# Kernel tuning notes

Hardware: AMD Instinct MI355X
Metric: run time of the kernel (lower is better)

## Reference

```python
import jax, jax.numpy as jnp
import numpy as np

H = 1024
NH = 16
DH = H // NH
EPS = 1e-12


def _heads(x):
    # [B,T,H] -> [B,NH,T,DH]
    B, T, _ = x.shape
    return x.reshape(B, T, NH, DH).transpose(0, 2, 1, 3)


def _layernorm(x, g, b):
    mu = jnp.mean(x, axis=-1, keepdims=True)
    var = jnp.mean(jnp.square(x - mu), axis=-1, keepdims=True)
    return (x - mu) * jax.lax.rsqrt(var + EPS) * g + b


def setup_inputs() -> dict:
    key = jax.random.key(0)
    ks = jax.random.split(key, 24)
    B, Tw, Te = 4, 1024, 128
    s = 0.02
    inp = {
        "word_hidden_states": jax.random.normal(ks[0], (B, Tw, H), jnp.float32),
        "entity_hidden_states": jax.random.normal(ks[1], (B, Te, H), jnp.float32),
        "attention_mask": jnp.zeros((B, 1, 1, Tw + Te), jnp.float32),
        "query_pos": jax.random.normal(ks[2], (B, Te, H), jnp.float32),
    }
    names = ["Wq", "Wk", "Wv", "Weq", "Wek", "Wev", "Wo", "Weo"]
    for i, n in enumerate(names):
        inp[n] = jax.random.normal(ks[3 + i], (H, H), jnp.float32) * s
        inp["b" + n[1:]] = jnp.zeros((H,), jnp.float32)
    inp["ln_g"] = jnp.ones((H,), jnp.float32)
    inp["ln_b"] = jnp.zeros((H,), jnp.float32)
    inp["eln_g"] = jnp.ones((H,), jnp.float32)
    inp["eln_b"] = jnp.zeros((H,), jnp.float32)
    return inp


def reference(word_hidden_states, entity_hidden_states, attention_mask, query_pos,
              Wq, bq, Wk, bk, Wv, bv, Weq, beq, Wek, bek, Wev, bev,
              Wo, bo, Weo, beo, ln_g, ln_b, eln_g, eln_b):
    Tw = word_hidden_states.shape[1]
    pos_ent = (entity_hidden_states + query_pos) * 0.5

    # per-stream projections (entity stream has its own e2w projections)
    qw = _heads(word_hidden_states @ Wq + bq)      # [B,NH,Tw,DH]
    qe = _heads(pos_ent @ Weq + beq)               # [B,NH,Te,DH]
    kw = _heads(word_hidden_states @ Wk + bk)
    ke = _heads(pos_ent @ Wek + bek)
    vw = _heads(word_hidden_states @ Wv + bv)
    ve = _heads(entity_hidden_states @ Wev + bev)  # value uses raw entity states

    q = jnp.concatenate([qw, qe], axis=2)          # [B,NH,T,DH]
    k = jnp.concatenate([kw, ke], axis=2)
    v = jnp.concatenate([vw, ve], axis=2)

    scores = jnp.einsum("bhqd,bhkd->bhqk", q, k) / np.sqrt(DH).astype(np.float32)
    scores = scores + attention_mask
    probs = jax.nn.softmax(scores, axis=-1)
    ctx = jnp.einsum("bhqk,bhkd->bhqd", probs, v)  # [B,NH,T,DH]
    B, _, T, _ = ctx.shape
    ctx = ctx.transpose(0, 2, 1, 3).reshape(B, T, H)

    word_self = ctx[:, :Tw, :]
    ent_self = ctx[:, Tw:, :]

    word_out = _layernorm(word_self @ Wo + bo + word_hidden_states, ln_g, ln_b)
    ent_out = _layernorm(ent_self @ Weo + beo + entity_hidden_states, eln_g, eln_b)
    return (word_out, ent_out)
```

## Files before the change

### kernel.cpp

```cpp
#include <hip/hip_runtime.h>
#include <math.h>

#define H_DIM 1024
#define NHEAD 16
#define DHEAD 64
#define T_W 1024
#define T_E 128
#define T_T 1152
#define BATCH 4

typedef __attribute__((ext_vector_type(8))) short s8b;
typedef __attribute__((ext_vector_type(4))) short s4b;
typedef __attribute__((ext_vector_type(4))) float f32x4;

__device__ __forceinline__ unsigned short f2bf(float f) {
    unsigned int u = __float_as_uint(f);
    u = (u + 0x7fffu + ((u >> 16) & 1u)) >> 16;
    return (unsigned short)u;
}

__device__ __forceinline__ void gld_lds16(const void* g, void* l) {
    __builtin_amdgcn_global_load_lds(
        (const __attribute__((address_space(1))) unsigned int*)g,
        (__attribute__((address_space(3))) unsigned int*)l, 16, 0, 0);
}

__global__ __launch_bounds__(256) void k_prep(const float* __restrict__ word,
                                              const float* __restrict__ ent,
                                              const float* __restrict__ qp,
                                              unsigned short* __restrict__ word_bf,
                                              unsigned short* __restrict__ pe_bf,
                                              unsigned short* __restrict__ ent_bf) {
    const int bid = blockIdx.x;
    if (bid < 4096) {
        int i = bid * 256 + threadIdx.x;
        float4 v = ((const float4*)word)[i];
        s4b o; o[0] = (short)f2bf(v.x); o[1] = (short)f2bf(v.y);
        o[2] = (short)f2bf(v.z); o[3] = (short)f2bf(v.w);
        *(s4b*)(word_bf + (size_t)i * 4) = o;
    } else {
        int i = (bid - 4096) * 256 + threadIdx.x;
        float4 a = ((const float4*)ent)[i];
        float4 b = ((const float4*)qp)[i];
        s4b e; e[0] = (short)f2bf(a.x); e[1] = (short)f2bf(a.y);
        e[2] = (short)f2bf(a.z); e[3] = (short)f2bf(a.w);
        *(s4b*)(ent_bf + (size_t)i * 4) = e;
        s4b p;
        p[0] = (short)f2bf((a.x + b.x) * 0.5f);
        p[1] = (short)f2bf((a.y + b.y) * 0.5f);
        p[2] = (short)f2bf((a.z + b.z) * 0.5f);
        p[3] = (short)f2bf((a.w + b.w) * 0.5f);
        *(s4b*)(pe_bf + (size_t)i * 4) = p;
    }
}

struct WPtrs { const float* w[8]; };
__global__ __launch_bounds__(256) void k_wT8(WPtrs ws, unsigned short* __restrict__ dstall) {
    __shared__ float tile[32][33];
    const float* src = ws.w[blockIdx.z];
    unsigned short* dst = dstall + (size_t)blockIdx.z * H_DIM * H_DIM;
    const int tx = threadIdx.x & 31, ty = threadIdx.x >> 5;
    const int kb = blockIdx.x * 32, nb = blockIdx.y * 32;
    #pragma unroll
    for (int i = 0; i < 4; i++)
        tile[ty * 4 + i][tx] = src[(size_t)(kb + ty * 4 + i) * H_DIM + nb + tx];
    __syncthreads();
    #pragma unroll
    for (int i = 0; i < 4; i++)
        dst[(size_t)(nb + ty * 4 + i) * H_DIM + kb + tx] = f2bf(tile[tx][ty * 4 + i]);
}

struct B3 { const float* b[3]; };
struct O3 { void* o[3]; };

__global__ __launch_bounds__(256) void k_proj(
    const unsigned short* __restrict__ A0, const unsigned short* __restrict__ A2,
    const unsigned short* __restrict__ Wtbase, B3 biases, O3 outs,
    int Tseq, int toff)
{
    const int z = blockIdx.z;
    const unsigned short* A = (z == 2) ? A2 : A0;
    const unsigned short* B = Wtbase + (size_t)z * H_DIM * H_DIM;
    const float* bias = biases.b[z];
    void* outp = outs.o[z];

    __shared__ unsigned short sm[8192];
    const int t = threadIdx.x;
    const int w = t >> 6, lane = t & 63;
    const int col = lane & 15, quad = lane >> 4;
    const int m0 = blockIdx.y * 128, n0 = blockIdx.x * 128;
    const int wm = w & 1, wn = w >> 1;
    const int rA = t >> 2, kA = (t & 3) * 8;

    f32x4 acc[4][4] = {};

    const unsigned short* gA0 = A + (size_t)(m0 + rA) * H_DIM + kA;
    const unsigned short* gA1 = A + (size_t)(m0 + 64 + rA) * H_DIM + kA;
    const unsigned short* gB0 = B + (size_t)(n0 + rA) * H_DIM + kA;
    const unsigned short* gB1 = B + (size_t)(n0 + 64 + rA) * H_DIM + kA;
    unsigned short* lA0 = &sm[t * 8];
    unsigned short* lA1 = &sm[2048 + t * 8];
    unsigned short* lB0 = &sm[4096 + t * 8];
    unsigned short* lB1 = &sm[6144 + t * 8];

    for (int k0 = 0; k0 < H_DIM; k0 += 32) {
        gld_lds16(gA0 + k0, lA0);
        gld_lds16(gA1 + k0, lA1);
        gld_lds16(gB0 + k0, lB0);
        gld_lds16(gB1 + k0, lB1);
        __syncthreads();
        s8b af[4], bfr[4];
        #pragma unroll
        for (int mt = 0; mt < 4; mt++)
            af[mt] = *(const s8b*)&sm[(wm * 64 + mt * 16 + col) * 32 + quad * 8];
        #pragma unroll
        for (int nt = 0; nt < 4; nt++)
            bfr[nt] = *(const s8b*)&sm[4096 + (wn * 64 + nt * 16 + col) * 32 + quad * 8];
        #pragma unroll
        for (int mt = 0; mt < 4; mt++)
            #pragma unroll
            for (int nt = 0; nt < 4; nt++)
                acc[mt][nt] = __builtin_amdgcn_mfma_f32_16x16x32_bf16(
                    af[mt], bfr[nt], acc[mt][nt], 0, 0, 0);
        __syncthreads();
    }

    #pragma unroll
    for (int mt = 0; mt < 4; mt++) {
        const int mg = m0 + wm * 64 + mt * 16 + quad * 4;
        const int b = mg / Tseq, tt = toff + (mg % Tseq);
        #pragma unroll
        for (int nt = 0; nt < 4; nt++) {
            const int ng = n0 + wn * 64 + nt * 16 + col;
            f32x4 c = acc[mt][nt];
            const float bn = bias[ng];
            if (z < 2) {
                unsigned short* out = (unsigned short*)outp;
                #pragma unroll
                for (int r = 0; r < 4; r++)
                    out[((size_t)b * T_T + tt + r) * H_DIM + ng] = f2bf(c[r] + bn);
            } else {
                unsigned short* out = (unsigned short*)outp;
                #pragma unroll
                for (int r = 0; r < 4; r++)
                    out[((size_t)b * H_DIM + ng) * T_T + tt + r] = f2bf(c[r] + bn);
            }
        }
    }
}

__global__ __launch_bounds__(256) void k_gemm_out(
    const unsigned short* __restrict__ ctx,
    const unsigned short* __restrict__ Wt_o, const unsigned short* __restrict__ Wt_eo,
    const float* __restrict__ bo, const float* __restrict__ beo,
    const float* __restrict__ word, const float* __restrict__ ent,
    float* __restrict__ out_word, float* __restrict__ out_ent)
{
    const int blk = blockIdx.x;
    const bool is_word = blk < 256;
    const int lb = is_word ? blk : blk - 256;
    const int m0 = (lb >> 3) * 128, n0 = (lb & 7) * 128;
    const unsigned short* B = is_word ? Wt_o : Wt_eo;
    const float* bias = is_word ? bo : beo;
    const float* resid = is_word ? word : ent;
    float* out = is_word ? out_word : out_ent;
    const int Tseq = is_word ? T_W : T_E;
    const int toff = is_word ? 0 : T_W;

    __shared__ unsigned short sm[8192];
    const int t = threadIdx.x;
    const int w = t >> 6, lane = t & 63;
    const int col = lane & 15, quad = lane >> 4;
    const int wm = w & 1, wn = w >> 1;
    const int rA = t >> 2, kA = (t & 3) * 8;

    f32x4 acc[4][4] = {};

    const int r0 = m0 + rA, r1 = m0 + 64 + rA;
    const size_t arow0 = (size_t)(r0 / Tseq) * T_T + toff + (r0 % Tseq);
    const size_t arow1 = (size_t)(r1 / Tseq) * T_T + toff + (r1 % Tseq);
    const unsigned short* gA0 = ctx + arow0 * H_DIM + kA;
    const unsigned short* gA1 = ctx + arow1 * H_DIM + kA;
    const unsigned short* gB0 = B + (size_t)(n0 + rA) * H_DIM + kA;
    const unsigned short* gB1 = B + (size_t)(n0 + 64 + rA) * H_DIM + kA;
    unsigned short* lA0 = &sm[t * 8];
    unsigned short* lA1 = &sm[2048 + t * 8];
    unsigned short* lB0 = &sm[4096 + t * 8];
    unsigned short* lB1 = &sm[6144 + t * 8];

    for (int k0 = 0; k0 < H_DIM; k0 += 32) {
        gld_lds16(gA0 + k0, lA0);
        gld_lds16(gA1 + k0, lA1);
        gld_lds16(gB0 + k0, lB0);
        gld_lds16(gB1 + k0, lB1);
        __syncthreads();
        s8b af[4], bfr[4];
        #pragma unroll
        for (int mt = 0; mt < 4; mt++)
            af[mt] = *(const s8b*)&sm[(wm * 64 + mt * 16 + col) * 32 + quad * 8];
        #pragma unroll
        for (int nt = 0; nt < 4; nt++)
            bfr[nt] = *(const s8b*)&sm[4096 + (wn * 64 + nt * 16 + col) * 32 + quad * 8];
        #pragma unroll
        for (int mt = 0; mt < 4; mt++)
            #pragma unroll
            for (int nt = 0; nt < 4; nt++)
                acc[mt][nt] = __builtin_amdgcn_mfma_f32_16x16x32_bf16(
                    af[mt], bfr[nt], acc[mt][nt], 0, 0, 0);
        __syncthreads();
    }

    #pragma unroll
    for (int mt = 0; mt < 4; mt++) {
        const int mg = m0 + wm * 64 + mt * 16 + quad * 4;
        #pragma unroll
        for (int nt = 0; nt < 4; nt++) {
            const int ng = n0 + wn * 64 + nt * 16 + col;
            f32x4 c = acc[mt][nt];
            const float bn = bias[ng];
            #pragma unroll
            for (int r = 0; r < 4; r++) {
                const size_t idx = (size_t)(mg + r) * H_DIM + ng;
                out[idx] = c[r] + bn + resid[idx];
            }
        }
    }
}

__global__ __launch_bounds__(256) void k_attn(
    const unsigned short* __restrict__ q, const unsigned short* __restrict__ k,
    const unsigned short* __restrict__ vt, const float* __restrict__ mask,
    unsigned short* __restrict__ ctx)
{
    const int tid = threadIdx.x;
    const int w = tid >> 6, lane = tid & 63;
    const int col = lane & 15, quad = lane >> 4;
    const int bh = blockIdx.x / 18;
    const int q0 = (blockIdx.x % 18) * 64 + w * 16;
    const int b = bh >> 4, h = bh & 15;

    __shared__ unsigned short sK[2][64 * 64];
    __shared__ unsigned short sV[2][64 * 64];
    __shared__ __align__(16) unsigned short sP[4][16 * 64];
    unsigned short* sp = &sP[w][0];

    const unsigned short* qp = q + ((size_t)b * T_T + q0) * H_DIM + h * DHEAD;
    const unsigned short* kp = k + (size_t)b * T_T * H_DIM + h * DHEAD;
    const unsigned short* vp = vt + ((size_t)b * H_DIM + h * DHEAD) * T_T;
    const float* mp = mask + (size_t)b * T_T;

    const s8b qf0 = *(const s8b*)(qp + (size_t)col * H_DIM + quad * 8);
    const s8b qf1 = *(const s8b*)(qp + (size_t)col * H_DIM + 32 + quad * 8);

    const int rA = tid >> 3;
    const int cA = (tid & 7) ^ (rA & 7);

    f32x4 O[4] = {};
    float m_c = -1e30f, l_c = 0.f;

    #define PREFETCH(J0, BUF)                                                        \
        {                                                                            \
            unsigned short* dK = &sK[BUF][0];                                        \
            unsigned short* dV = &sV[BUF][0];                                        \
            gld_lds16(kp + (size_t)((J0) + rA) * H_DIM + cA * 8, dK + tid * 8);      \
            gld_lds16(kp + (size_t)((J0) + rA + 32) * H_DIM + cA * 8,                \
                      dK + (256 + tid) * 8);                                         \
            gld_lds16(vp + (size_t)rA * T_T + (J0) + cA * 8, dV + tid * 8);          \
            gld_lds16(vp + (size_t)(rA + 32) * T_T + (J0) + cA * 8,                  \
                      dV + (256 + tid) * 8);                                         \
        }

    PREFETCH(0, 0)
    for (int it = 0; it < 18; it++) {
        const int j0 = it * 64;
        __syncthreads();
        if (it < 17) PREFETCH(j0 + 64, (it + 1) & 1)
        const unsigned short* K0 = &sK[it & 1][0];
        const unsigned short* V0 = &sV[it & 1][0];

        float s[16];
        float mx = -1e30f;
        #pragma unroll
        for (int kt = 0; kt < 4; kt++) {
            const int rk = kt * 16 + col;
            const int csw = quad ^ (rk & 7);
            s8b k0f = *(const s8b*)(K0 + rk * 64 + csw * 8);
            s8b k1f = *(const s8b*)(K0 + rk * 64 + (csw ^ 4) * 8);
            f32x4 z = {0.f, 0.f, 0.f, 0.f};
            z = __builtin_amdgcn_mfma_f32_16x16x32_bf16(k0f, qf0, z, 0, 0, 0);
            z = __builtin_amdgcn_mfma_f32_16x16x32_bf16(k1f, qf1, z, 0, 0, 0);
            float4 mv = *(const float4*)(mp + j0 + kt * 16 + quad * 4);
            float mvv[4] = {mv.x, mv.y, mv.z, mv.w};
            #pragma unroll
            for (int r = 0; r < 4; r++) {
                float sv = z[r] * 0.125f + mvv[r];
                s[kt * 4 + r] = sv;
                mx = fmaxf(mx, sv);
            }
        }
        mx = fmaxf(mx, __shfl_xor(mx, 16));
        mx = fmaxf(mx, __shfl_xor(mx, 32));
        const float mnew = fmaxf(m_c, mx);
        float rs = 0.f;
        unsigned short pb[16];
        #pragma unroll
        for (int i = 0; i < 16; i++) {
            float p = __expf(s[i] - mnew);
            rs += p;
            pb[i] = f2bf(p);
        }
        rs += __shfl_xor(rs, 16);
        rs += __shfl_xor(rs, 32);
        if (__all(mnew == m_c)) {
            l_c += rs;
        } else {
            const float alpha = __expf(m_c - mnew);
            l_c = l_c * alpha + rs;
            #pragma unroll
            for (int dt = 0; dt < 4; dt++)
                #pragma unroll
                for (int r = 0; r < 4; r++) O[dt][r] *= alpha;
        }
        m_c = mnew;

        #pragma unroll
        for (int kt = 0; kt < 4; kt++) {
            s4b pv; pv[0] = pb[kt * 4]; pv[1] = pb[kt * 4 + 1];
            pv[2] = pb[kt * 4 + 2]; pv[3] = pb[kt * 4 + 3];
            const int chunk = 2 * kt + (quad >> 1);
            *(s4b*)(sp + col * 64 + ((chunk ^ (col & 7)) * 8) + (quad & 1) * 4) = pv;
        }
        const s8b p0 = *(const s8b*)(sp + col * 64 + ((quad ^ (col & 7)) * 8));
        const s8b p1 = *(const s8b*)(sp + col * 64 + (((4 + quad) ^ (col & 7)) * 8));

        #pragma unroll
        for (int dt = 0; dt < 4; dt++) {
            const int rf = dt * 16 + col;
            const int csw = quad ^ (rf & 7);
            s8b v0 = *(const s8b*)(V0 + rf * 64 + csw * 8);
            s8b v1 = *(const s8b*)(V0 + rf * 64 + (csw ^ 4) * 8);
            O[dt] = __builtin_amdgcn_mfma_f32_16x16x32_bf16(v0, p0, O[dt], 0, 0, 0);
            O[dt] = __builtin_amdgcn_mfma_f32_16x16x32_bf16(v1, p1, O[dt], 0, 0, 0);
        }
    }
    #undef PREFETCH

    const float inv = 1.f / l_c;
    unsigned short* ob = ctx + ((size_t)b * T_T + q0 + col) * H_DIM + h * DHEAD;
    #pragma unroll
    for (int dt = 0; dt < 4; dt++) {
        s4b o;
        #pragma unroll
        for (int r = 0; r < 4; r++) o[r] = (short)f2bf(O[dt][r] * inv);
        *(s4b*)(ob + dt * 16 + quad * 4) = o;
    }
}

__global__ __launch_bounds__(256) void k_layernorm(float* __restrict__ x,
                                                   const float* __restrict__ g0,
                                                   const float* __restrict__ b0,
                                                   const float* __restrict__ g1,
                                                   const float* __restrict__ b1)
{
    const int row = blockIdx.x;
    const float* g = row < 4096 ? g0 : g1;
    const float* bta = row < 4096 ? b0 : b1;
    float* p = x + (size_t)row * H_DIM;
    const int t = threadIdx.x;
    float vals[4];
    float s = 0.f, ss = 0.f;
    #pragma unroll
    for (int i = 0; i < 4; i++) {
        float v = p[t + 256 * i];
        vals[i] = v;
        s += v;
        ss += v * v;
    }
    #pragma unroll
    for (int o = 32; o > 0; o >>= 1) {
        s += __shfl_xor(s, o);
        ss += __shfl_xor(ss, o);
    }
    __shared__ float red[2][4];
    const int wid = t >> 6, lane = t & 63;
    if (lane == 0) { red[0][wid] = s; red[1][wid] = ss; }
    __syncthreads();
    s = red[0][0] + red[0][1] + red[0][2] + red[0][3];
    ss = red[1][0] + red[1][1] + red[1][2] + red[1][3];
    float mu = s * (1.0f / H_DIM);
    float var = ss * (1.0f / H_DIM) - mu * mu;
    float r = rsqrtf(var + 1e-12f);
    #pragma unroll
    for (int i = 0; i < 4; i++) {
        int idx = t + 256 * i;
        p[idx] = (vals[i] - mu) * r * g[idx] + bta[idx];
    }
}

extern "C" void kernel_launch(void* const* d_in, const int* in_sizes, int n_in,
                              void* d_out, int out_size, void* d_ws, size_t ws_size,
                              hipStream_t stream) {
    const float* word = (const float*)d_in[0];
    const float* ent  = (const float*)d_in[1];
    const float* mask = (const float*)d_in[2];
    const float* qpos = (const float*)d_in[3];
    const float* Wq  = (const float*)d_in[4];  const float* bq  = (const float*)d_in[5];
    const float* Wk  = (const float*)d_in[6];  const float* bk  = (const float*)d_in[7];
    const float* Wv  = (const float*)d_in[8];  const float* bv  = (const float*)d_in[9];
    const float* Weq = (const float*)d_in[10]; const float* beq = (const float*)d_in[11];
    const float* Wek = (const float*)d_in[12]; const float* bek = (const float*)d_in[13];
    const float* Wev = (const float*)d_in[14]; const float* bev = (const float*)d_in[15];
    const float* Wo  = (const float*)d_in[16]; const float* bo  = (const float*)d_in[17];
    const float* Weo = (const float*)d_in[18]; const float* beo = (const float*)d_in[19];
    const float* ln_g  = (const float*)d_in[20]; const float* ln_b  = (const float*)d_in[21];
    const float* eln_g = (const float*)d_in[22]; const float* eln_b = (const float*)d_in[23];

    char* ws = (char*)d_ws;
    unsigned short* word_bf = (unsigned short*)(ws);
    unsigned short* pe_bf   = (unsigned short*)(ws + 8388608);
    unsigned short* ent_bf  = (unsigned short*)(ws + 9437184);
    unsigned short* Wt      = (unsigned short*)(ws + 10485760);
    unsigned short* qb      = (unsigned short*)(ws + 27262976);
    unsigned short* kb      = (unsigned short*)(ws + 36700160);
    unsigned short* vt      = (unsigned short*)(ws + 46137344);
    unsigned short* ctx     = (unsigned short*)(ws + 55574528);

    float* out_word = (float*)d_out;
    float* out_ent  = out_word + 4194304;

    const size_t WSZ = (size_t)H_DIM * H_DIM;
    unsigned short* Wt_q  = Wt;
    unsigned short* Wt_eq = Wt + 3 * WSZ;
    unsigned short* Wt_o  = Wt + 6 * WSZ;
    unsigned short* Wt_eo = Wt + 7 * WSZ;

    k_prep<<<dim3(4608), 256, 0, stream>>>(word, ent, qpos, word_bf, pe_bf, ent_bf);

    WPtrs wp = {{Wq, Wk, Wv, Weq, Wek, Wev, Wo, Weo}};
    k_wT8<<<dim3(32, 32, 8), 256, 0, stream>>>(wp, Wt);

    B3 bw = {{bq, bk, bv}};
    O3 ow = {{qb, kb, vt}};
    k_proj<<<dim3(8, 32, 3), 256, 0, stream>>>(word_bf, word_bf, Wt_q, bw, ow, T_W, 0);
    B3 be = {{beq, bek, bev}};
    k_proj<<<dim3(8, 4, 3), 256, 0, stream>>>(pe_bf, ent_bf, Wt_eq, be, ow, T_E, T_W);

    k_attn<<<dim3(NHEAD * BATCH * 18), 256, 0, stream>>>(qb, kb, vt, mask, ctx);

    k_gemm_out<<<dim3(288), 256, 0, stream>>>(ctx, Wt_o, Wt_eo, bo, beo,
                                              word, ent, out_word, out_ent);

    k_layernorm<<<dim3(4608), 256, 0, stream>>>(out_word, ln_g, ln_b, eln_g, eln_b);
}
```

Baseline: 302.7 us.

## Merge word/entity projection launches, use packed bf16 converts and exp2 softmax

Merges the two projection launches into one 8x36x3 grid that picks the word or entity input and weights by block row, which removes a launch and the small under-filled entity grid. It also replaces the scalar bf16 rounding with packed cvt_pk_bf16 conversions in prep, the V-transpose stores, the attention P tile and the output. The softmax now folds the scale and log2e into a single FMA and uses hardware exp2. The packed builtin may round differently from the manual round-to-nearest-even, and mask values are scaled by log2e.

```diff
diff --git a/kernel.cpp b/kernel.cpp
--- a/kernel.cpp
+++ b/kernel.cpp
@@ -13,10 +13,30 @@
 typedef __attribute__((ext_vector_type(4))) short s4b;
 typedef __attribute__((ext_vector_type(4))) float f32x4;
 
+#define LOG2E 1.44269504088896f
+
 __device__ __forceinline__ unsigned short f2bf(float f) {
     unsigned int u = __float_as_uint(f);
     u = (u + 0x7fffu + ((u >> 16) & 1u)) >> 16;
     return (unsigned short)u;
+}
+
+__device__ __forceinline__ unsigned int pk_bf16(float a, float b) {
+#if __has_builtin(__builtin_amdgcn_cvt_pk_bf16_f32)
+    typedef __bf16 bf2 __attribute__((ext_vector_type(2)));
+    bf2 r = __builtin_amdgcn_cvt_pk_bf16_f32(a, b);
+    return __builtin_bit_cast(unsigned int, r);
+#else
+    return (unsigned int)f2bf(a) | ((unsigned int)f2bf(b) << 16);
+#endif
+}
+
+__device__ __forceinline__ float exp2f_fast(float x) {
+#if __has_builtin(__builtin_amdgcn_exp2f)
+    return __builtin_amdgcn_exp2f(x);
+#else
+    return exp2f(x);
+#endif
 }
 
 __device__ __forceinline__ void gld_lds16(const void* g, void* l) {
@@ -35,22 +55,17 @@
     if (bid < 4096) {
         int i = bid * 256 + threadIdx.x;
         float4 v = ((const float4*)word)[i];
-        s4b o; o[0] = (short)f2bf(v.x); o[1] = (short)f2bf(v.y);
-        o[2] = (short)f2bf(v.z); o[3] = (short)f2bf(v.w);
-        *(s4b*)(word_bf + (size_t)i * 4) = o;
+        unsigned int lo = pk_bf16(v.x, v.y), hi = pk_bf16(v.z, v.w);
+        *(uint2*)(word_bf + (size_t)i * 4) = make_uint2(lo, hi);
     } else {
         int i = (bid - 4096) * 256 + threadIdx.x;
         float4 a = ((const float4*)ent)[i];
         float4 b = ((const float4*)qp)[i];
-        s4b e; e[0] = (short)f2bf(a.x); e[1] = (short)f2bf(a.y);
-        e[2] = (short)f2bf(a.z); e[3] = (short)f2bf(a.w);
-        *(s4b*)(ent_bf + (size_t)i * 4) = e;
-        s4b p;
-        p[0] = (short)f2bf((a.x + b.x) * 0.5f);
-        p[1] = (short)f2bf((a.y + b.y) * 0.5f);
-        p[2] = (short)f2bf((a.z + b.z) * 0.5f);
-        p[3] = (short)f2bf((a.w + b.w) * 0.5f);
-        *(s4b*)(pe_bf + (size_t)i * 4) = p;
+        *(uint2*)(ent_bf + (size_t)i * 4) =
+            make_uint2(pk_bf16(a.x, a.y), pk_bf16(a.z, a.w));
+        *(uint2*)(pe_bf + (size_t)i * 4) =
+            make_uint2(pk_bf16((a.x + b.x) * 0.5f, (a.y + b.y) * 0.5f),
+                       pk_bf16((a.z + b.z) * 0.5f, (a.w + b.w) * 0.5f));
     }
 }
 
@@ -70,25 +85,31 @@
         dst[(size_t)(nb + ty * 4 + i) * H_DIM + kb + tx] = f2bf(tile[tx][ty * 4 + i]);
 }
 
-struct B3 { const float* b[3]; };
-struct O3 { void* o[3]; };
+struct B6 { const float* b[6]; };
+struct O3p { void* o[3]; };
 
 __global__ __launch_bounds__(256) void k_proj(
-    const unsigned short* __restrict__ A0, const unsigned short* __restrict__ A2,
-    const unsigned short* __restrict__ Wtbase, B3 biases, O3 outs,
-    int Tseq, int toff)
+    const unsigned short* __restrict__ word_bf,
+    const unsigned short* __restrict__ pe_bf,
+    const unsigned short* __restrict__ ent_bf,
+    const unsigned short* __restrict__ Wtbase, B6 biases, O3p outs)
 {
     const int z = blockIdx.z;
-    const unsigned short* A = (z == 2) ? A2 : A0;
-    const unsigned short* B = Wtbase + (size_t)z * H_DIM * H_DIM;
-    const float* bias = biases.b[z];
+    const bool isw = blockIdx.y < 32;
+    const int Tseq = isw ? T_W : T_E;
+    const int toff = isw ? 0 : T_W;
+    const int m0 = (isw ? blockIdx.y : (blockIdx.y - 32)) * 128;
+    const unsigned short* A = isw ? word_bf : (z == 2 ? ent_bf : pe_bf);
+    const int wi = (isw ? 0 : 3) + z;
+    const unsigned short* B = Wtbase + (size_t)wi * H_DIM * H_DIM;
+    const float* bias = biases.b[wi];
     void* outp = outs.o[z];
 
     __shared__ unsigned short sm[8192];
     const int t = threadIdx.x;
     const int w = t >> 6, lane = t & 63;
     const int col = lane & 15, quad = lane >> 4;
-    const int m0 = blockIdx.y * 128, n0 = blockIdx.x * 128;
+    const int n0 = blockIdx.x * 128;
     const int wm = w & 1, wn = w >> 1;
     const int rA = t >> 2, kA = (t & 3) * 8;
 
@@ -141,9 +162,9 @@
                     out[((size_t)b * T_T + tt + r) * H_DIM + ng] = f2bf(c[r] + bn);
             } else {
                 unsigned short* out = (unsigned short*)outp;
-                #pragma unroll
-                for (int r = 0; r < 4; r++)
-                    out[((size_t)b * H_DIM + ng) * T_T + tt + r] = f2bf(c[r] + bn);
+                *(uint2*)(out + ((size_t)b * H_DIM + ng) * T_T + tt) =
+                    make_uint2(pk_bf16(c[0] + bn, c[1] + bn),
+                               pk_bf16(c[2] + bn, c[3] + bn));
             }
         }
     }
@@ -255,6 +276,8 @@
     const int rA = tid >> 3;
     const int cA = (tid & 7) ^ (rA & 7);
 
+    const float SC2 = 0.125f * LOG2E;
+
     f32x4 O[4] = {};
     float m_c = -1e30f, l_c = 0.f;
 
@@ -290,10 +313,10 @@
             z = __builtin_amdgcn_mfma_f32_16x16x32_bf16(k0f, qf0, z, 0, 0, 0);
             z = __builtin_amdgcn_mfma_f32_16x16x32_bf16(k1f, qf1, z, 0, 0, 0);
             float4 mv = *(const float4*)(mp + j0 + kt * 16 + quad * 4);
-            float mvv[4] = {mv.x, mv.y, mv.z, mv.w};
+            float mvv[4] = {mv.x * LOG2E, mv.y * LOG2E, mv.z * LOG2E, mv.w * LOG2E};
             #pragma unroll
             for (int r = 0; r < 4; r++) {
-                float sv = z[r] * 0.125f + mvv[r];
+                float sv = fmaf(z[r], SC2, mvv[r]);
                 s[kt * 4 + r] = sv;
                 mx = fmaxf(mx, sv);
             }
@@ -301,20 +324,19 @@
         mx = fmaxf(mx, __shfl_xor(mx, 16));
         mx = fmaxf(mx, __shfl_xor(mx, 32));
         const float mnew = fmaxf(m_c, mx);
+        float p[16];
         float rs = 0.f;
-        unsigned short pb[16];
         #pragma unroll
         for (int i = 0; i < 16; i++) {
-            float p = __expf(s[i] - mnew);
-            rs += p;
-            pb[i] = f2bf(p);
+            p[i] = exp2f_fast(s[i] - mnew);
+            rs += p[i];
         }
         rs += __shfl_xor(rs, 16);
         rs += __shfl_xor(rs, 32);
         if (__all(mnew == m_c)) {
             l_c += rs;
         } else {
-            const float alpha = __expf(m_c - mnew);
+            const float alpha = exp2f_fast(m_c - mnew);
             l_c = l_c * alpha + rs;
             #pragma unroll
             for (int dt = 0; dt < 4; dt++)
@@ -323,12 +345,14 @@
         }
         m_c = mnew;
 
+        unsigned int d[8];
+        #pragma unroll
+        for (int i = 0; i < 8; i++) d[i] = pk_bf16(p[2 * i], p[2 * i + 1]);
         #pragma unroll
         for (int kt = 0; kt < 4; kt++) {
-            s4b pv; pv[0] = pb[kt * 4]; pv[1] = pb[kt * 4 + 1];
-            pv[2] = pb[kt * 4 + 2]; pv[3] = pb[kt * 4 + 3];
             const int chunk = 2 * kt + (quad >> 1);
-            *(s4b*)(sp + col * 64 + ((chunk ^ (col & 7)) * 8) + (quad & 1) * 4) = pv;
+            *(uint2*)(sp + col * 64 + ((chunk ^ (col & 7)) * 8) + (quad & 1) * 4) =
+                make_uint2(d[2 * kt], d[2 * kt + 1]);
         }
         const s8b p0 = *(const s8b*)(sp + col * 64 + ((quad ^ (col & 7)) * 8));
         const s8b p1 = *(const s8b*)(sp + col * 64 + (((4 + quad) ^ (col & 7)) * 8));
@@ -349,10 +373,9 @@
     unsigned short* ob = ctx + ((size_t)b * T_T + q0 + col) * H_DIM + h * DHEAD;
     #pragma unroll
     for (int dt = 0; dt < 4; dt++) {
-        s4b o;
-        #pragma unroll
-        for (int r = 0; r < 4; r++) o[r] = (short)f2bf(O[dt][r] * inv);
-        *(s4b*)(ob + dt * 16 + quad * 4) = o;
+        *(uint2*)(ob + dt * 16 + quad * 4) =
+            make_uint2(pk_bf16(O[dt][0] * inv, O[dt][1] * inv),
+                       pk_bf16(O[dt][2] * inv, O[dt][3] * inv));
     }
 }
 
@@ -429,8 +452,6 @@
     float* out_ent  = out_word + 4194304;
 
     const size_t WSZ = (size_t)H_DIM * H_DIM;
-    unsigned short* Wt_q  = Wt;
-    unsigned short* Wt_eq = Wt + 3 * WSZ;
     unsigned short* Wt_o  = Wt + 6 * WSZ;
     unsigned short* Wt_eo = Wt + 7 * WSZ;
 
@@ -439,11 +460,9 @@
     WPtrs wp = {{Wq, Wk, Wv, Weq, Wek, Wev, Wo, Weo}};
     k_wT8<<<dim3(32, 32, 8), 256, 0, stream>>>(wp, Wt);
 
-    B3 bw = {{bq, bk, bv}};
-    O3 ow = {{qb, kb, vt}};
-    k_proj<<<dim3(8, 32, 3), 256, 0, stream>>>(word_bf, word_bf, Wt_q, bw, ow, T_W, 0);
-    B3 be = {{beq, bek, bev}};
-    k_proj<<<dim3(8, 4, 3), 256, 0, stream>>>(pe_bf, ent_bf, Wt_eq, be, ow, T_E, T_W);
+    B6 bb = {{bq, bk, bv, beq, bek, bev}};
+    O3p ow = {{qb, kb, vt}};
+    k_proj<<<dim3(8, 36, 3), 256, 0, stream>>>(word_bf, pe_bf, ent_bf, Wt, bb, ow);
 
     k_attn<<<dim3(NHEAD * BATCH * 18), 256, 0, stream>>>(qb, kb, vt, mask, ctx);
 
```

New measurement: 291.4 us. -3.7%, faster.
